# Optimization experiments

Measured on AMD Instinct MI355X. Metric: run time of the kernel, lower is better.

## Reference

```python
import jax, jax.numpy as jnp
import numpy as np

L, D, F, H = 4, 1024, 2048, 8
DH = D // H
EPS = 1e-5


def setup_inputs() -> dict:
    key = jax.random.key(0)
    ks = jax.random.split(key, 8)
    B, S = 4, 1024
    sd = 1.0 / np.sqrt(D)
    sf = 1.0 / np.sqrt(F)
    return {
        "X": jax.random.normal(ks[0], (B, S, D), jnp.float32),
        "Wq": jax.random.normal(ks[1], (L, D, D), jnp.float32) * sd,
        "Wk": jax.random.normal(ks[2], (L, D, D), jnp.float32) * sd,
        "Wv": jax.random.normal(ks[3], (L, D, D), jnp.float32) * sd,
        "Wg": jax.random.normal(ks[4], (L, D, D), jnp.float32) * sd,
        "Wo": jax.random.normal(ks[5], (L, D, D), jnp.float32) * sd,
        "W1": jax.random.normal(ks[6], (L, D, F), jnp.float32) * sd,
        "W2": jax.random.normal(ks[7], (L, F, D), jnp.float32) * sf,
        "ln_scale": jnp.ones((D,), jnp.float32),
        "ln_bias": jnp.zeros((D,), jnp.float32),
        "gn_scale": jnp.ones((L, D), jnp.float32),
        "gn_bias": jnp.zeros((L, D), jnp.float32),
    }


def _layer_norm(x, scale, bias):
    mu = x.mean(-1, keepdims=True)
    var = x.var(-1, keepdims=True)
    return (x - mu) * jax.lax.rsqrt(var + EPS) * scale + bias


def _rotate(x, cos, sin):
    # x: (B,S,H,DH); cos/sin: (1,S,1,DH//2); rotary pairs (even, odd)
    x1, x2 = x[..., 0::2], x[..., 1::2]
    r1 = x1 * cos - x2 * sin
    r2 = x1 * sin + x2 * cos
    return jnp.stack([r1, r2], axis=-1).reshape(x.shape)


def _decay_matrix(S):
    # D[h,n,m] = gamma_h^(n-m) for n>=m else 0
    gammas = 1.0 - jnp.exp(jnp.linspace(np.log(1 / 32), np.log(1 / 512), H)).astype(jnp.float32)
    n = jnp.arange(S)
    diff = (n[:, None] - n[None, :]).astype(jnp.float32)
    pw = jnp.exp(jnp.clip(diff, 0.0)[None] * jnp.log(gammas)[:, None, None])
    return jnp.where(diff[None] >= 0, pw, 0.0)  # (H,S,S)


def _retention(x, Wq, Wk, Wv, Wg, Wo, gn_s, gn_b, Dm, cos, sin):
    B, S, _ = x.shape
    Q = (x @ Wq).reshape(B, S, H, DH)
    K = (x @ Wk).reshape(B, S, H, DH)
    V = (x @ Wv).reshape(B, S, H, DH)
    Q = _rotate(Q, cos, sin)
    K = _rotate(K, cos, -sin)  # conjugate phase
    att = jnp.einsum('bnhd,bmhd->bhnm', Q, K) * Dm  # (B,H,S,S)
    Y = jnp.einsum('bhnm,bmhd->bnhd', att, V)
    # group norm: normalize each head's output per token
    mu = Y.mean(-1, keepdims=True)
    var = Y.var(-1, keepdims=True)
    Y = (Y - mu) * jax.lax.rsqrt(var + EPS)
    Y = Y.reshape(B, S, D) * gn_s + gn_b
    G = jax.nn.swish(x @ Wg)
    return (G * Y) @ Wo


def reference(X, Wq, Wk, Wv, Wg, Wo, W1, W2, ln_scale, ln_bias, gn_scale, gn_bias):
    B, S, _ = X.shape
    pos = jnp.arange(S, dtype=jnp.float32)
    inv_freq = 1.0 / (10000.0 ** (jnp.arange(0, DH, 2, dtype=jnp.float32) / DH))
    ang = pos[:, None] * inv_freq[None, :]  # (S, DH//2)
    cos = jnp.cos(ang)[None, :, None, :]
    sin = jnp.sin(ang)[None, :, None, :]
    Dm = _decay_matrix(S)
    for i in range(L):
        Yr = _retention(_layer_norm(X, ln_scale, ln_bias), Wq[i], Wk[i], Wv[i],
                        Wg[i], Wo[i], gn_scale[i], gn_bias[i], Dm, cos, sin) + X
        X = jax.nn.gelu(_layer_norm(Yr, ln_scale, ln_bias) @ W1[i]) @ W2[i] + Yr
    return X
```

## Files before the change

kernel.cpp:

```cpp
#include <hip/hip_runtime.h>
#include <hip/hip_bf16.h>
#include <cmath>

#define LAYERS 4
#define Bb 4
#define Ss 1024
#define Dd 1024
#define Ff 2048
#define Hh 8
#define DHd 128
#define Mm (Bb * Ss)
#define EPSf 1e-5f
#define LDQ 4096

typedef __attribute__((ext_vector_type(8))) short short8v;
typedef __attribute__((ext_vector_type(4))) float f32x4;
typedef __attribute__((ext_vector_type(4))) unsigned int u32x4;

__device__ __forceinline__ float swish_f(float x) { return x / (1.f + expf(-x)); }
__device__ __forceinline__ float gelu_f(float x) {
  return 0.5f * x * (1.f + tanhf(0.7978845608028654f * (x + 0.044715f * x * x * x)));
}
__device__ __forceinline__ unsigned short f2bfu(float f) {
  __hip_bfloat16 h = __float2bfloat16(f);
  return __builtin_bit_cast(unsigned short, h);
}
__device__ __forceinline__ float bfu2f(unsigned short u) {
  unsigned v = ((unsigned)u) << 16;
  return __builtin_bit_cast(float, v);
}
__device__ __forceinline__ void gl_lds16(const void* g, void* l) {
  __builtin_amdgcn_global_load_lds((__attribute__((address_space(1))) void*)g,
                                   (__attribute__((address_space(3))) void*)l, 16, 0, 0);
}
__device__ __forceinline__ f32x4 mfma16(short8v a, short8v b, f32x4 c) {
  return __builtin_amdgcn_mfma_f32_16x16x32_bf16(a, b, c, 0, 0, 0);
}

__global__ __launch_bounds__(256) void ln_bf16_kernel(const float* __restrict__ x,
                                                      short* __restrict__ outb,
                                                      const float* __restrict__ sc,
                                                      const float* __restrict__ bi) {
  const int row = blockIdx.x;
  const int t = threadIdx.x;
  const float4 v = *(const float4*)(x + (size_t)row * Dd + t * 4);
  float s = v.x + v.y + v.z + v.w;
  float s2 = v.x * v.x + v.y * v.y + v.z * v.z + v.w * v.w;
#pragma unroll
  for (int o = 32; o > 0; o >>= 1) { s += __shfl_down(s, o); s2 += __shfl_down(s2, o); }
  __shared__ float ps[4], ps2[4];
  if ((t & 63) == 0) { ps[t >> 6] = s; ps2[t >> 6] = s2; }
  __syncthreads();
  s = ps[0] + ps[1] + ps[2] + ps[3];
  s2 = ps2[0] + ps2[1] + ps2[2] + ps2[3];
  const float mu = s * (1.f / Dd);
  const float var = s2 * (1.f / Dd) - mu * mu;
  const float rstd = rsqrtf(var + EPSf);
  const float4 g = *(const float4*)(sc + t * 4);
  const float4 b = *(const float4*)(bi + t * 4);
  const float o0 = (v.x - mu) * rstd * g.x + b.x;
  const float o1 = (v.y - mu) * rstd * g.y + b.y;
  const float o2 = (v.z - mu) * rstd * g.z + b.z;
  const float o3 = (v.w - mu) * rstd * g.w + b.w;
  unsigned p0 = (unsigned)f2bfu(o0) | ((unsigned)f2bfu(o1) << 16);
  unsigned p1 = (unsigned)f2bfu(o2) | ((unsigned)f2bfu(o3) << 16);
  uint2 pk; pk.x = p0; pk.y = p1;
  *(uint2*)(outb + (size_t)row * Dd + t * 4) = pk;
}

__global__ void rope_table_kernel(float* __restrict__ ct, float* __restrict__ st) {
  const int i = blockIdx.x * 256 + threadIdx.x;
  const int s = i >> 6, f = i & 63;
  const float inv = powf(10000.f, -(float)f / 64.f);
  const float a = (float)s * inv;
  ct[i] = cosf(a);
  st[i] = sinf(a);
}

__global__ __launch_bounds__(256) void wtrans_all_kernel(
    const float* __restrict__ Wq, const float* __restrict__ Wk,
    const float* __restrict__ Wv, const float* __restrict__ Wg,
    const float* __restrict__ Wo, const float* __restrict__ W1,
    const float* __restrict__ W2,
    short* __restrict__ Wqkvgt, short* __restrict__ Wot,
    short* __restrict__ W1t, short* __restrict__ W2t) {
  __shared__ float tile[32][33];
  const int t = threadIdx.x;
  const int tc = t & 31, tr8 = t >> 5;
  const int blk = blockIdx.x;
  const float* src; short* dst; int K, N, n0, k0, nl;
  if (blk < 4096) {
    const int bx = blk & 127, ky = blk >> 7;
    n0 = bx * 32; k0 = ky * 32;
    const int which = n0 >> 10;
    src = (which == 0) ? Wq : (which == 1) ? Wk : (which == 2) ? Wv : Wg;
    nl = n0 & 1023; N = 1024; K = 1024; dst = Wqkvgt;
  } else if (blk < 5120) {
    const int b2 = blk - 4096;
    n0 = (b2 & 31) * 32; k0 = (b2 >> 5) * 32; nl = n0;
    src = Wo; N = 1024; K = 1024; dst = Wot;
  } else if (blk < 7168) {
    const int b2 = blk - 5120;
    n0 = (b2 & 63) * 32; k0 = (b2 >> 6) * 32; nl = n0;
    src = W1; N = 2048; K = 1024; dst = W1t;
  } else {
    const int b2 = blk - 7168;
    n0 = (b2 & 31) * 32; k0 = (b2 >> 5) * 32; nl = n0;
    src = W2; N = 1024; K = 2048; dst = W2t;
  }
#pragma unroll
  for (int i = 0; i < 4; ++i) {
    const int r = tr8 + i * 8;
    tile[r][tc] = src[(size_t)(k0 + r) * N + nl + tc];
  }
  __syncthreads();
#pragma unroll
  for (int i = 0; i < 4; ++i) {
    const int r = tr8 + i * 8;
    dst[(size_t)(n0 + r) * K + k0 + tc] = (short)f2bfu(tile[tc][r]);
  }
}

__global__ __launch_bounds__(256) void rvt_kernel(short* __restrict__ QKVGb,
                                                  short* __restrict__ Vt,
                                                  const float* __restrict__ ct,
                                                  const float* __restrict__ st) {
  __shared__ short tile[32][33];
  const int blk = blockIdx.x, t = threadIdx.x;
  if (blk < 8192) {
    const int idx = blk * 256 + t;
    const int f = idx & 63;
    const int h = (idx >> 6) & 7;
    const int r = idx >> 9;
    const int s = r & (Ss - 1);
    const float c = ct[(s << 6) + f], sn = st[(s << 6) + f];
    const size_t qo = (size_t)r * LDQ + h * DHd + 2 * f;
    const unsigned qp = *(const unsigned*)(QKVGb + qo);
    const unsigned kp = *(const unsigned*)(QKVGb + qo + 1024);
    const float qx = bfu2f((unsigned short)(qp & 0xffff)), qy = bfu2f((unsigned short)(qp >> 16));
    const float kx = bfu2f((unsigned short)(kp & 0xffff)), ky = bfu2f((unsigned short)(kp >> 16));
    const unsigned qn = (unsigned)f2bfu(qx * c - qy * sn) |
                        ((unsigned)f2bfu(qx * sn + qy * c) << 16);
    const unsigned kn = (unsigned)f2bfu(kx * c + ky * sn) |
                        ((unsigned)f2bfu(-kx * sn + ky * c) << 16);
    *(unsigned*)(QKVGb + qo) = qn;
    *(unsigned*)(QKVGb + qo + 1024) = kn;
  } else {
    const int vb = blk - 8192;
    const int s0 = (vb & 31) * 32, d0 = ((vb >> 5) & 3) * 32, bh = vb >> 7;
    const int bb = bh >> 3, h = bh & 7;
    const int tc = t & 31, tr8 = t >> 5;
#pragma unroll
    for (int i = 0; i < 4; ++i) {
      const int r = tr8 + i * 8;
      tile[r][tc] = QKVGb[(size_t)(bb * Ss + s0 + r) * LDQ + 2048 + h * DHd + d0 + tc];
    }
    __syncthreads();
#pragma unroll
    for (int i = 0; i < 4; ++i) {
      const int r = tr8 + i * 8;
      Vt[(size_t)(bh * DHd + d0 + r) * Ss + s0 + tc] = tile[tc][r];
    }
  }
}

template <int EPI>
__global__ __launch_bounds__(512, 2) void gemm14(const short* __restrict__ A,
                                                 const short* __restrict__ Bt,
                                                 float* __restrict__ Cf,
                                                 short* __restrict__ Cb,
                                                 const float* __restrict__ Res,
                                                 int N, int K, int ldc) {
  __shared__ __align__(16) short As[2][2][128 * 64];
  __shared__ __align__(16) short Bs[2][2][128 * 64];
  const int t = threadIdx.x;
  const int w = t >> 6, l = t & 63;
  const int lq = l >> 4, lr = l & 15;
  const int wr = w >> 2, wc = w & 3;
  const int bhalf = wc >> 1, brow0 = (wc & 1) * 64;
  const int nwg = gridDim.x * gridDim.y;
  const int bid0 = blockIdx.x + blockIdx.y * gridDim.x;
  const int lgid = (bid0 & 7) * (nwg >> 3) + (bid0 >> 3);
  const int bx = lgid % gridDim.x, by = lgid / gridDim.x;
  const int row0 = by * 256, col0 = bx * 256;
  const int NT = K >> 6;

  f32x4 acc[8][4] = {};
  short8v a[4][2], b[4][2];

  auto stageA = [&](int kt, int hf) {
    const int db = kt & 1;
#pragma unroll
    for (int i = 0; i < 2; ++i) {
      const int c = t + i * 512;
      const int row = c >> 3, slot = c & 7;
      gl_lds16(A + (size_t)(row0 + hf * 128 + row) * K + kt * 64 + ((slot ^ (row & 7)) << 3),
               &As[db][hf][c * 8]);
    }
  };
  auto stageB = [&](int kt, int hf) {
    const int db = kt & 1;
#pragma unroll
    for (int i = 0; i < 2; ++i) {
      const int c = t + i * 512;
      const int row = c >> 3, slot = c & 7;
      gl_lds16(Bt + (size_t)(col0 + hf * 128 + row) * K + kt * 64 + ((slot ^ (row & 7)) << 3),
               &Bs[db][hf][c * 8]);
    }
  };
  auto rdA = [&](int db, int m, int ks) -> short8v {
    const int row = m * 16 + lr;
    return *(const short8v*)&As[db][wr][row * 64 + (((ks << 2) + lq) ^ (row & 7)) * 8];
  };
  auto rdB = [&](int db, int n, int ks) -> short8v {
    const int row = brow0 + n * 16 + lr;
    return *(const short8v*)&Bs[db][bhalf][row * 64 + (((ks << 2) + lq) ^ (row & 7)) * 8];
  };

  stageA(0, 0); stageA(0, 1); stageB(0, 0); stageB(0, 1);
  if (NT > 1) { stageB(1, 0); stageB(1, 1); }
  if (NT > 1) { asm volatile("s_waitcnt vmcnt(4)" ::: "memory"); }
  else        { asm volatile("s_waitcnt vmcnt(0)" ::: "memory"); }
  asm volatile("s_barrier" ::: "memory");

  for (int kt = 0; kt < NT; ++kt) {
    const int db = kt & 1;
#pragma unroll
    for (int m = 0; m < 4; ++m) a[m][0] = rdA(db, m, 0);
#pragma unroll
    for (int n = 0; n < 4; ++n) b[n][0] = rdB(db, n, 0);
    if (kt + 1 < NT) stageA(kt + 1, 0);
    __builtin_amdgcn_s_setprio(1);
#pragma unroll
    for (int m = 0; m < 4; ++m)
#pragma unroll
      for (int n = 0; n < 4; ++n) acc[m][n] = mfma16(a[m][0], b[n][0], acc[m][n]);
    __builtin_amdgcn_s_setprio(0);
    asm volatile("s_barrier" ::: "memory");
#pragma unroll
    for (int m = 0; m < 4; ++m) a[m][1] = rdA(db, m, 1);
#pragma unroll
    for (int n = 0; n < 4; ++n) b[n][1] = rdB(db, n, 1);
    if (kt + 1 < NT) stageA(kt + 1, 1);
    __builtin_amdgcn_s_setprio(1);
#pragma unroll
    for (int m = 0; m < 4; ++m)
#pragma unroll
      for (int n = 0; n < 4; ++n) acc[m][n] = mfma16(a[m][1], b[n][1], acc[m][n]);
    __builtin_amdgcn_s_setprio(0);
    asm volatile("s_barrier" ::: "memory");
#pragma unroll
    for (int m = 0; m < 4; ++m) a[m][0] = rdA(db, m + 4, 0);
    if (kt + 2 < NT) { stageB(kt + 2, 0); stageB(kt + 2, 1); }
    __builtin_amdgcn_s_setprio(1);
#pragma unroll
    for (int m = 0; m < 4; ++m)
#pragma unroll
      for (int n = 0; n < 4; ++n) acc[m + 4][n] = mfma16(a[m][0], b[n][0], acc[m + 4][n]);
    __builtin_amdgcn_s_setprio(0);
    asm volatile("s_barrier" ::: "memory");
#pragma unroll
    for (int m = 0; m < 4; ++m) a[m][1] = rdA(db, m + 4, 1);
    __builtin_amdgcn_s_setprio(1);
#pragma unroll
    for (int m = 0; m < 4; ++m)
#pragma unroll
      for (int n = 0; n < 4; ++n) acc[m + 4][n] = mfma16(a[m][1], b[n][1], acc[m + 4][n]);
    __builtin_amdgcn_s_setprio(0);
    if (kt + 2 < NT) { asm volatile("s_waitcnt vmcnt(4)" ::: "memory"); }
    else             { asm volatile("s_waitcnt vmcnt(0)" ::: "memory"); }
    asm volatile("s_barrier" ::: "memory");
  }

#pragma unroll
  for (int m = 0; m < 8; ++m) {
#pragma unroll
    for (int n = 0; n < 4; ++n) {
#pragma unroll
      for (int r = 0; r < 4; ++r) {
        const int row = row0 + wr * 128 + m * 16 + lq * 4 + r;
        const int col = col0 + wc * 64 + n * 16 + lr;
        const size_t o = (size_t)row * ldc + col;
        float v = acc[m][n][r];
        if (EPI == 0) Cb[o] = (short)f2bfu(v);
        else if (EPI == 1) Cf[o] = v + Res[o];
        else Cb[o] = (short)f2bfu(gelu_f(v));
      }
    }
  }
}

template <int EPI>
__global__ __launch_bounds__(512) void gemm11(const short* __restrict__ A,
                                              const short* __restrict__ Bt,
                                              float* __restrict__ Cf,
                                              short* __restrict__ Cb,
                                              const float* __restrict__ Res,
                                              int K, int lda, int ldb, int ldc, int nxt) {
  __shared__ __align__(16) short As[3][256 * 64];
  __shared__ __align__(16) short Bs[3][128 * 64];
  const int t = threadIdx.x;
  const int w = t >> 6, l = t & 63;
  const int lq = l >> 4, lr = l & 15;
  const int wr = w >> 2, wc = w & 3;
  const int nwg = gridDim.x;
  const int lgid = (blockIdx.x & 7) * (nwg >> 3) + (blockIdx.x >> 3);
  const int mt = lgid / nxt, nt_ = lgid % nxt;
  const int row0 = mt * 256, col0 = nt_ * 128;
  const int NT = K >> 6;
  f32x4 acc[8][2] = {};
  short8v a[4][2], b[2][2];

  auto stageA = [&](int kt, int hf) {
    const int s = kt % 3;
#pragma unroll
    for (int i = 0; i < 2; ++i) {
      const int c = t + i * 512;
      const int row = c >> 3, slot = c & 7;
      gl_lds16(A + (size_t)(row0 + hf * 128 + row) * lda + kt * 64 + ((slot ^ (row & 7)) << 3),
               &As[s][hf * 8192 + c * 8]);
    }
  };
  auto stageB = [&](int kt) {
    const int s = kt % 3;
#pragma unroll
    for (int i = 0; i < 2; ++i) {
      const int c = t + i * 512;
      const int row = c >> 3, slot = c & 7;
      gl_lds16(Bt + (size_t)(col0 + row) * ldb + kt * 64 + ((slot ^ (row & 7)) << 3),
               &Bs[s][c * 8]);
    }
  };
  auto rdA = [&](int s, int m, int ks) -> short8v {
    const int row = wr * 128 + m * 16 + lr;
    return *(const short8v*)&As[s][row * 64 + (((ks << 2) + lq) ^ (row & 7)) * 8];
  };
  auto rdB = [&](int s, int n, int ks) -> short8v {
    const int row = wc * 32 + n * 16 + lr;
    return *(const short8v*)&Bs[s][row * 64 + (((ks << 2) + lq) ^ (row & 7)) * 8];
  };

  stageA(0, 0); stageA(0, 1); stageB(0);
  stageA(1, 0); stageA(1, 1); stageB(1);
  asm volatile("s_waitcnt vmcnt(6)" ::: "memory");
  asm volatile("s_barrier" ::: "memory");

  for (int kt = 0; kt < NT; ++kt) {
    const int s = kt % 3;
#pragma unroll
    for (int m = 0; m < 4; ++m) { a[m][0] = rdA(s, m, 0); a[m][1] = rdA(s, m, 1); }
#pragma unroll
    for (int n = 0; n < 2; ++n) { b[n][0] = rdB(s, n, 0); b[n][1] = rdB(s, n, 1); }
    if (kt + 2 < NT) stageA(kt + 2, 0);
    __builtin_amdgcn_s_setprio(1);
#pragma unroll
    for (int m = 0; m < 4; ++m)
#pragma unroll
      for (int n = 0; n < 2; ++n) {
        acc[m][n] = mfma16(a[m][0], b[n][0], acc[m][n]);
        acc[m][n] = mfma16(a[m][1], b[n][1], acc[m][n]);
      }
    __builtin_amdgcn_s_setprio(0);
    asm volatile("s_barrier" ::: "memory");
#pragma unroll
    for (int m = 0; m < 4; ++m) { a[m][0] = rdA(s, m + 4, 0); a[m][1] = rdA(s, m + 4, 1); }
    if (kt + 2 < NT) { stageA(kt + 2, 1); stageB(kt + 2); }
    __builtin_amdgcn_s_setprio(1);
#pragma unroll
    for (int m = 0; m < 4; ++m)
#pragma unroll
      for (int n = 0; n < 2; ++n) {
        acc[m + 4][n] = mfma16(a[m][0], b[n][0], acc[m + 4][n]);
        acc[m + 4][n] = mfma16(a[m][1], b[n][1], acc[m + 4][n]);
      }
    __builtin_amdgcn_s_setprio(0);
    if (kt + 2 < NT) { asm volatile("s_waitcnt vmcnt(6)" ::: "memory"); }
    else             { asm volatile("s_waitcnt vmcnt(0)" ::: "memory"); }
    asm volatile("s_barrier" ::: "memory");
  }

#pragma unroll
  for (int m = 0; m < 8; ++m) {
#pragma unroll
    for (int n = 0; n < 2; ++n) {
#pragma unroll
      for (int r = 0; r < 4; ++r) {
        const int row = row0 + wr * 128 + m * 16 + lq * 4 + r;
        const int col = col0 + wc * 32 + n * 16 + lr;
        const size_t o = (size_t)row * ldc + col;
        float v = acc[m][n][r];
        if (EPI == 0) Cb[o] = (short)f2bfu(v);
        else if (EPI == 1) Cf[o] = v + Res[o];
        else Cb[o] = (short)f2bfu(gelu_f(v));
      }
    }
  }
}

template <int EPI>
__global__ __launch_bounds__(512) void gemm12(const short* __restrict__ A,
                                              const short* __restrict__ Bt,
                                              float* __restrict__ Cf,
                                              short* __restrict__ Cb,
                                              const float* __restrict__ Res,
                                              int K, int lda, int ldb, int ldc, int nxt) {
  __shared__ __align__(16) short As[3][128 * 64];
  __shared__ __align__(16) short Bs[3][128 * 64];
  const int t = threadIdx.x;
  const int w = t >> 6, l = t & 63;
  const int lq = l >> 4, lr = l & 15;
  const int wr = w >> 2, wc = w & 3;
  const int nwg = gridDim.x;
  const int lgid = (blockIdx.x & 7) * (nwg >> 3) + (blockIdx.x >> 3);
  const int mt = lgid / nxt, nt_ = lgid % nxt;
  const int row0 = mt * 128, col0 = nt_ * 128;
  const int NT = K >> 6;
  f32x4 acc[4][2] = {};
  short8v a[4][2], b[2][2];

  auto stageA = [&](int kt) {
    const int s = kt % 3;
#pragma unroll
    for (int i = 0; i < 2; ++i) {
      const int c = t + i * 512;
      const int row = c >> 3, slot = c & 7;
      gl_lds16(A + (size_t)(row0 + row) * lda + kt * 64 + ((slot ^ (row & 7)) << 3),
               &As[s][c * 8]);
    }
  };
  auto stageB = [&](int kt) {
    const int s = kt % 3;
#pragma unroll
    for (int i = 0; i < 2; ++i) {
      const int c = t + i * 512;
      const int row = c >> 3, slot = c & 7;
      gl_lds16(Bt + (size_t)(col0 + row) * ldb + kt * 64 + ((slot ^ (row & 7)) << 3),
               &Bs[s][c * 8]);
    }
  };
  auto rdA = [&](int s, int m, int ks) -> short8v {
    const int row = wr * 64 + m * 16 + lr;
    return *(const short8v*)&As[s][row * 64 + (((ks << 2) + lq) ^ (row & 7)) * 8];
  };
  auto rdB = [&](int s, int n, int ks) -> short8v {
    const int row = wc * 32 + n * 16 + lr;
    return *(const short8v*)&Bs[s][row * 64 + (((ks << 2) + lq) ^ (row & 7)) * 8];
  };

  stageA(0); stageB(0);
  stageA(1); stageB(1);
  asm volatile("s_waitcnt vmcnt(4)" ::: "memory");
  asm volatile("s_barrier" ::: "memory");

  for (int kt = 0; kt < NT; ++kt) {
    const int s = kt % 3;
#pragma unroll
    for (int m = 0; m < 4; ++m) { a[m][0] = rdA(s, m, 0); a[m][1] = rdA(s, m, 1); }
#pragma unroll
    for (int n = 0; n < 2; ++n) { b[n][0] = rdB(s, n, 0); b[n][1] = rdB(s, n, 1); }
    if (kt + 2 < NT) stageA(kt + 2);
    __builtin_amdgcn_s_setprio(1);
#pragma unroll
    for (int m = 0; m < 2; ++m)
#pragma unroll
      for (int n = 0; n < 2; ++n) {
        acc[m][n] = mfma16(a[m][0], b[n][0], acc[m][n]);
        acc[m][n] = mfma16(a[m][1], b[n][1], acc[m][n]);
      }
    __builtin_amdgcn_s_setprio(0);
    asm volatile("s_barrier" ::: "memory");
    if (kt + 2 < NT) stageB(kt + 2);
    __builtin_amdgcn_s_setprio(1);
#pragma unroll
    for (int m = 2; m < 4; ++m)
#pragma unroll
      for (int n = 0; n < 2; ++n) {
        acc[m][n] = mfma16(a[m][0], b[n][0], acc[m][n]);
        acc[m][n] = mfma16(a[m][1], b[n][1], acc[m][n]);
      }
    __builtin_amdgcn_s_setprio(0);
    if (kt + 2 < NT) { asm volatile("s_waitcnt vmcnt(4)" ::: "memory"); }
    else             { asm volatile("s_waitcnt vmcnt(0)" ::: "memory"); }
    asm volatile("s_barrier" ::: "memory");
  }

#pragma unroll
  for (int m = 0; m < 4; ++m) {
#pragma unroll
    for (int n = 0; n < 2; ++n) {
#pragma unroll
      for (int r = 0; r < 4; ++r) {
        const int row = row0 + wr * 64 + m * 16 + lq * 4 + r;
        const int col = col0 + wc * 32 + n * 16 + lr;
        const size_t o = (size_t)row * ldc + col;
        float v = acc[m][n][r];
        if (EPI == 0) Cb[o] = (short)f2bfu(v);
        else if (EPI == 1) Cf[o] = v + Res[o];
        else Cb[o] = (short)f2bfu(gelu_f(v));
      }
    }
  }
}

__global__ __launch_bounds__(256) void ret4_kernel(const short* __restrict__ QKb,
                                                   const short* __restrict__ Vt,
                                                   float* __restrict__ Y0,
                                                   float* __restrict__ Y1) {
  __shared__ __align__(16) short Ks[2][64 * 128];
  __shared__ __align__(16) short Vs[2][128 * 64];
  const int t = threadIdx.x, w = t >> 6, l = t & 63;
  const int lq = l >> 4, lr = l & 15;
  const int u = blockIdx.x;
  const int lgid = (u & 7) * 64 + (u >> 3);
  const int half = lgid >> 8;
  const int rest = lgid & 255;
  const int bh = rest >> 3, j = rest & 7;
  const int qb = half ? j : 7 - j;
  const int b = bh >> 3, h = bh & 7;
  const int q0 = qb * 128;
  const float lstep = (logf(1.f / 512.f) - logf(1.f / 32.f)) * (1.f / 7.f);
  const float gamma = 1.f - expf(logf(1.f / 32.f) + (float)h * lstep);
  const float l2g = logf(gamma) * 1.44269504f;
  const short* Qp = QKb;
  const short* Kp = QKb + 1024;

  short8v qf[2][4];
#pragma unroll
  for (int qn = 0; qn < 2; ++qn)
#pragma unroll
    for (int ks = 0; ks < 4; ++ks)
      qf[qn][ks] = *(const short8v*)(Qp + (size_t)(b * Ss + q0 + w * 32 + qn * 16 + lr) * LDQ +
                                     h * DHd + ks * 32 + lq * 8);

  float cmf[4], csr[4];
#pragma unroll
  for (int mf = 0; mf < 4; ++mf) cmf[mf] = exp2f(l2g * (float)(-16 * mf));
#pragma unroll
  for (int r = 0; r < 4; ++r) csr[r] = exp2f(l2g * (float)(63 - 4 * lq - r));

  f32x4 yacc[2][8] = {};
  const int nt = 2 * qb + 2;
  const int sb = ((lq & 1) * 2) * 16 + lr;

  auto stageKV = [&](int m0, int buf) {
#pragma unroll
    for (int i = 0; i < 4; ++i) {
      const int c = (w * 4 + i) * 64 + l;
      const int row = c >> 4, slot = c & 15;
      gl_lds16(Kp + (size_t)(b * Ss + m0 + row) * LDQ + h * DHd + ((slot ^ (row & 7)) * 8),
               &Ks[buf][(w * 4 + i) * 512]);
    }
#pragma unroll
    for (int i = 0; i < 4; ++i) {
      const int c = (w * 4 + i) * 64 + l;
      const int row = c >> 3, slot = c & 7;
      gl_lds16(Vt + (size_t)(bh * DHd + row) * Ss + m0 + ((slot ^ (row & 7)) * 8),
               &Vs[buf][(w * 4 + i) * 512]);
    }
  };

  stageKV(half * 64, 0);
  __syncthreads();
  int cur = 0;
  for (int tt = half; tt < nt; tt += 2) {
    const int m0 = tt * 64;
    if (tt + 2 < nt) stageKV((tt + 2) * 64, cur ^ 1);

    f32x4 st[4][2] = {};
    __builtin_amdgcn_s_setprio(1);
#pragma unroll
    for (int mf = 0; mf < 4; ++mf) {
      const int row = mf * 16 + lr;
#pragma unroll
      for (int ks = 0; ks < 4; ++ks) {
        short8v kf = *(const short8v*)&Ks[cur][row * 128 + (((4 * ks + lq) ^ (row & 7)) * 8)];
        st[mf][0] = mfma16(kf, qf[0][ks], st[mf][0]);
        st[mf][1] = mfma16(kf, qf[1][ks], st[mf][1]);
      }
    }
    __builtin_amdgcn_s_setprio(0);
    float rs[2];
#pragma unroll
    for (int qn = 0; qn < 2; ++qn)
      rs[qn] = exp2f(l2g * (float)(q0 + w * 32 + qn * 16 + lr - m0 - 63));
#pragma unroll
    for (int mf = 0; mf < 4; ++mf)
#pragma unroll
      for (int qn = 0; qn < 2; ++qn)
#pragma unroll
        for (int r = 0; r < 4; ++r) {
          const int qg = q0 + w * 32 + qn * 16 + lr;
          const int kvg = m0 + mf * 16 + lq * 4 + r;
          const float wgt = (qg >= kvg) ? rs[qn] * cmf[mf] * csr[r] : 0.f;
          st[mf][qn][r] *= wgt;
        }
    unsigned pk[4][2][2];
#pragma unroll
    for (int mf = 0; mf < 4; ++mf)
#pragma unroll
      for (int qn = 0; qn < 2; ++qn)
#pragma unroll
        for (int p = 0; p < 2; ++p)
          pk[mf][qn][p] = (unsigned)f2bfu(st[mf][qn][2 * p]) |
                          ((unsigned)f2bfu(st[mf][qn][2 * p + 1]) << 16);
    short8v afr[2][2];
#pragma unroll
    for (int qn = 0; qn < 2; ++qn)
#pragma unroll
      for (int ks2 = 0; ks2 < 2; ++ks2) {
        u32x4 wd;
#pragma unroll
        for (int wj = 0; wj < 4; ++wj) {
          const int src = sb + (wj >> 1) * 16;
          const unsigned v0 = __shfl(pk[2 * ks2 + 0][qn][wj & 1], src);
          const unsigned v1 = __shfl(pk[2 * ks2 + 1][qn][wj & 1], src);
          wd[wj] = (lq >= 2) ? v1 : v0;
        }
        afr[qn][ks2] = __builtin_bit_cast(short8v, wd);
      }
    __builtin_amdgcn_s_setprio(1);
#pragma unroll
    for (int nd = 0; nd < 8; ++nd) {
      const int row = nd * 16 + lr;
#pragma unroll
      for (int ks2 = 0; ks2 < 2; ++ks2) {
        short8v vf = *(const short8v*)&Vs[cur][row * 64 + (((4 * ks2 + lq) ^ (row & 7)) * 8)];
        yacc[0][nd] = mfma16(afr[0][ks2], vf, yacc[0][nd]);
        yacc[1][nd] = mfma16(afr[1][ks2], vf, yacc[1][nd]);
      }
    }
    __builtin_amdgcn_s_setprio(0);
    __syncthreads();
    cur ^= 1;
  }
  float* Y = half ? Y1 : Y0;
#pragma unroll
  for (int qn = 0; qn < 2; ++qn)
#pragma unroll
    for (int r = 0; r < 4; ++r) {
      const int q = q0 + w * 32 + qn * 16 + lq * 4 + r;
#pragma unroll
      for (int nd = 0; nd < 8; ++nd)
        Y[(size_t)(b * Ss + q) * Dd + h * DHd + nd * 16 + lr] = yacc[qn][nd][r];
    }
}

__global__ __launch_bounds__(256) void gate_kernel(const float* __restrict__ Y0,
                                                   const float* __restrict__ Y1,
                                                   const short* __restrict__ Graw,
                                                   short* __restrict__ Gb,
                                                   const float* __restrict__ gs,
                                                   const float* __restrict__ gb) {
  const int lane = threadIdx.x & 63;
  const int rowh = blockIdx.x * 4 + (threadIdx.x >> 6);
  const int h = rowh & 7;
  const int row = rowh >> 3;
  const size_t ybase = (size_t)row * Dd + (size_t)h * DHd + lane * 2;
  float2 a = *(const float2*)(Y0 + ybase);
  const float2 c = *(const float2*)(Y1 + ybase);
  a.x += c.x; a.y += c.y;
  float s = a.x + a.y, s2 = a.x * a.x + a.y * a.y;
#pragma unroll
  for (int o = 32; o > 0; o >>= 1) { s += __shfl_down(s, o); s2 += __shfl_down(s2, o); }
  s = __shfl(s, 0);
  s2 = __shfl(s2, 0);
  const float mu = s * (1.f / DHd);
  const float rstd = rsqrtf(s2 * (1.f / DHd) - mu * mu + EPSf);
  const int d = h * DHd + lane * 2;
  const float2 g = *(const float2*)(gs + d);
  const float2 bbv = *(const float2*)(gb + d);
  const float y0 = (a.x - mu) * rstd * g.x + bbv.x;
  const float y1 = (a.y - mu) * rstd * g.y + bbv.y;
  const unsigned gr = *(const unsigned*)(Graw + (size_t)row * LDQ + 3072 + h * DHd + lane * 2);
  const float gx = bfu2f((unsigned short)(gr & 0xffff));
  const float gy = bfu2f((unsigned short)(gr >> 16));
  const unsigned o01 = (unsigned)f2bfu(swish_f(gx) * y0) |
                       ((unsigned)f2bfu(swish_f(gy) * y1) << 16);
  *(unsigned*)(Gb + ybase) = o01;
}

extern "C" void kernel_launch(void* const* d_in, const int* in_sizes, int n_in,
                              void* d_out, int out_size, void* d_ws, size_t ws_size,
                              hipStream_t stream) {
  const float* X = (const float*)d_in[0];
  const float* Wq = (const float*)d_in[1];
  const float* Wk = (const float*)d_in[2];
  const float* Wv = (const float*)d_in[3];
  const float* Wg = (const float*)d_in[4];
  const float* Wo = (const float*)d_in[5];
  const float* W1 = (const float*)d_in[6];
  const float* W2 = (const float*)d_in[7];
  const float* lns = (const float*)d_in[8];
  const float* lnb = (const float*)d_in[9];
  const float* gns = (const float*)d_in[10];
  const float* gnb = (const float*)d_in[11];
  float* out = (float*)d_out;

  char* W = (char*)d_ws;
  const size_t MB = 1u << 20;
  float* Abuf  = (float*)(W);
  short* Xnb   = (short*)(W + 16 * MB);
  short* QKVGb = (short*)(W + 24 * MB);
  float* Y0    = (float*)(W + 56 * MB);
  float* Y1    = (float*)(W + 72 * MB);
  short* Vtb   = (short*)(W + 88 * MB);
  short* Gb    = (short*)(W + 96 * MB);
  short* Wqkvgt= (short*)(W + 104 * MB);
  short* Wot   = (short*)(W + 112 * MB);
  short* W1t   = (short*)(W + 114 * MB);
  short* W2t   = (short*)(W + 118 * MB);
  float* ct    = (float*)(W + 122 * MB);
  float* st    = ct + Ss * 64;
  short* Hb = QKVGb;

  rope_table_kernel<<<(Ss * 64) / 256, 256, 0, stream>>>(ct, st);

  for (int l = 0; l < LAYERS; ++l) {
    const size_t DD = (size_t)Dd * Dd;
    const float* Acur = (l == 0) ? X : Abuf;
    wtrans_all_kernel<<<9216, 256, 0, stream>>>(Wq + l * DD, Wk + l * DD, Wv + l * DD,
                                                Wg + l * DD, Wo + l * DD,
                                                W1 + (size_t)l * Dd * Ff,
                                                W2 + (size_t)l * Ff * Dd,
                                                Wqkvgt, Wot, W1t, W2t);
    ln_bf16_kernel<<<Mm, 256, 0, stream>>>(Acur, Xnb, lns, lnb);
    gemm14<0><<<dim3(16, 16), 512, 0, stream>>>(Xnb, Wqkvgt, nullptr, QKVGb,
                                                nullptr, 4096, Dd, LDQ);
    rvt_kernel<<<12288, 256, 0, stream>>>(QKVGb, Vtb, ct, st);
    ret4_kernel<<<512, 256, 0, stream>>>(QKVGb, Vtb, Y0, Y1);
    gate_kernel<<<(Mm * Hh) / 4, 256, 0, stream>>>(Y0, Y1, QKVGb, Gb,
                                                   gns + (size_t)l * Dd, gnb + (size_t)l * Dd);
    gemm12<1><<<256, 512, 0, stream>>>(Gb, Wot, Abuf, nullptr, Acur,
                                       Dd, Dd, Dd, Dd, 8);
    ln_bf16_kernel<<<Mm, 256, 0, stream>>>(Abuf, Xnb, lns, lnb);
    gemm11<2><<<256, 512, 0, stream>>>(Xnb, W1t, nullptr, Hb, nullptr,
                                       Dd, Dd, Dd, Ff, 16);
    float* dst = (l == LAYERS - 1) ? out : Abuf;
    gemm12<1><<<256, 512, 0, stream>>>(Hb, W2t, dst, nullptr, Abuf,
                                       Ff, Ff, Ff, Dd, 8);
  }
}
```

Baseline: 746.7 us.

## Fuse retention with group-norm gating and add explicit barriers in QKVG GEMM

```diff
diff --git a/kernel.cpp b/kernel.cpp
--- a/kernel.cpp
+++ b/kernel.cpp
@@ -230,6 +230,9 @@
 #pragma unroll
     for (int n = 0; n < 4; ++n) b[n][0] = rdB(db, n, 0);
     if (kt + 1 < NT) stageA(kt + 1, 0);
+    asm volatile("s_barrier" ::: "memory");
+    asm volatile("s_waitcnt lgkmcnt(0)" ::: "memory");
+    __builtin_amdgcn_sched_barrier(0);
     __builtin_amdgcn_s_setprio(1);
 #pragma unroll
     for (int m = 0; m < 4; ++m)
@@ -242,6 +245,9 @@
 #pragma unroll
     for (int n = 0; n < 4; ++n) b[n][1] = rdB(db, n, 1);
     if (kt + 1 < NT) stageA(kt + 1, 1);
+    asm volatile("s_barrier" ::: "memory");
+    asm volatile("s_waitcnt lgkmcnt(0)" ::: "memory");
+    __builtin_amdgcn_sched_barrier(0);
     __builtin_amdgcn_s_setprio(1);
 #pragma unroll
     for (int m = 0; m < 4; ++m)
@@ -252,6 +258,9 @@
 #pragma unroll
     for (int m = 0; m < 4; ++m) a[m][0] = rdA(db, m + 4, 0);
     if (kt + 2 < NT) { stageB(kt + 2, 0); stageB(kt + 2, 1); }
+    asm volatile("s_barrier" ::: "memory");
+    asm volatile("s_waitcnt lgkmcnt(0)" ::: "memory");
+    __builtin_amdgcn_sched_barrier(0);
     __builtin_amdgcn_s_setprio(1);
 #pragma unroll
     for (int m = 0; m < 4; ++m)
@@ -261,6 +270,9 @@
     asm volatile("s_barrier" ::: "memory");
 #pragma unroll
     for (int m = 0; m < 4; ++m) a[m][1] = rdA(db, m + 4, 1);
+    asm volatile("s_barrier" ::: "memory");
+    asm volatile("s_waitcnt lgkmcnt(0)" ::: "memory");
+    __builtin_amdgcn_sched_barrier(0);
     __builtin_amdgcn_s_setprio(1);
 #pragma unroll
     for (int m = 0; m < 4; ++m)
@@ -502,44 +514,36 @@
   }
 }
 
-__global__ __launch_bounds__(256) void ret4_kernel(const short* __restrict__ QKb,
+__global__ __launch_bounds__(256) void ret5_kernel(const short* __restrict__ QKVGb,
                                                    const short* __restrict__ Vt,
-                                                   float* __restrict__ Y0,
-                                                   float* __restrict__ Y1) {
+                                                   short* __restrict__ Gb,
+                                                   const float* __restrict__ gs,
+                                                   const float* __restrict__ gb) {
   __shared__ __align__(16) short Ks[2][64 * 128];
   __shared__ __align__(16) short Vs[2][128 * 64];
   const int t = threadIdx.x, w = t >> 6, l = t & 63;
   const int lq = l >> 4, lr = l & 15;
   const int u = blockIdx.x;
-  const int lgid = (u & 7) * 64 + (u >> 3);
-  const int half = lgid >> 8;
-  const int rest = lgid & 255;
-  const int bh = rest >> 3, j = rest & 7;
-  const int qb = half ? j : 7 - j;
+  const int lgid = (u & 7) * 32 + (u >> 3);
+  const int bh = lgid >> 3, pr = lgid & 7;
   const int b = bh >> 3, h = bh & 7;
-  const int q0 = qb * 128;
   const float lstep = (logf(1.f / 512.f) - logf(1.f / 32.f)) * (1.f / 7.f);
   const float gamma = 1.f - expf(logf(1.f / 32.f) + (float)h * lstep);
   const float l2g = logf(gamma) * 1.44269504f;
-  const short* Qp = QKb;
-  const short* Kp = QKb + 1024;
-
-  short8v qf[2][4];
-#pragma unroll
-  for (int qn = 0; qn < 2; ++qn)
-#pragma unroll
-    for (int ks = 0; ks < 4; ++ks)
-      qf[qn][ks] = *(const short8v*)(Qp + (size_t)(b * Ss + q0 + w * 32 + qn * 16 + lr) * LDQ +
-                                     h * DHd + ks * 32 + lq * 8);
+  const short* Qp = QKVGb;
+  const short* Kp = QKVGb + 1024;
 
   float cmf[4], csr[4];
 #pragma unroll
   for (int mf = 0; mf < 4; ++mf) cmf[mf] = exp2f(l2g * (float)(-16 * mf));
 #pragma unroll
   for (int r = 0; r < 4; ++r) csr[r] = exp2f(l2g * (float)(63 - 4 * lq - r));
-
-  f32x4 yacc[2][8] = {};
-  const int nt = 2 * qb + 2;
+  float gsv[8], gbv[8];
+#pragma unroll
+  for (int nd = 0; nd < 8; ++nd) {
+    gsv[nd] = gs[h * DHd + nd * 16 + lr];
+    gbv[nd] = gb[h * DHd + nd * 16 + lr];
+  }
   const int sb = ((lq & 1) * 2) * 16 + lr;
 
   auto stageKV = [&](int m0, int buf) {
@@ -559,124 +563,103 @@
     }
   };
 
-  stageKV(half * 64, 0);
-  __syncthreads();
-  int cur = 0;
-  for (int tt = half; tt < nt; tt += 2) {
-    const int m0 = tt * 64;
-    if (tt + 2 < nt) stageKV((tt + 2) * 64, cur ^ 1);
-
-    f32x4 st[4][2] = {};
-    __builtin_amdgcn_s_setprio(1);
-#pragma unroll
-    for (int mf = 0; mf < 4; ++mf) {
-      const int row = mf * 16 + lr;
-#pragma unroll
-      for (int ks = 0; ks < 4; ++ks) {
-        short8v kf = *(const short8v*)&Ks[cur][row * 128 + (((4 * ks + lq) ^ (row & 7)) * 8)];
-        st[mf][0] = mfma16(kf, qf[0][ks], st[mf][0]);
-        st[mf][1] = mfma16(kf, qf[1][ks], st[mf][1]);
-      }
-    }
-    __builtin_amdgcn_s_setprio(0);
-    float rs[2];
-#pragma unroll
-    for (int qn = 0; qn < 2; ++qn)
-      rs[qn] = exp2f(l2g * (float)(q0 + w * 32 + qn * 16 + lr - m0 - 63));
-#pragma unroll
-    for (int mf = 0; mf < 4; ++mf)
-#pragma unroll
-      for (int qn = 0; qn < 2; ++qn)
+  for (int pass = 0; pass < 2; ++pass) {
+    const int qb = pass ? (15 - pr) : pr;
+    const int q0 = qb * 64;
+    const int nt = qb + 1;
+    short8v qf[4];
+#pragma unroll
+    for (int ks = 0; ks < 4; ++ks)
+      qf[ks] = *(const short8v*)(Qp + (size_t)(b * Ss + q0 + w * 16 + lr) * LDQ +
+                                 h * DHd + ks * 32 + lq * 8);
+    f32x4 yacc[8] = {};
+    stageKV(0, 0);
+    __syncthreads();
+    int cur = 0;
+    for (int tt = 0; tt < nt; ++tt) {
+      const int m0 = tt * 64;
+      if (tt + 1 < nt) stageKV((tt + 1) * 64, cur ^ 1);
+
+      f32x4 st[4] = {};
+      __builtin_amdgcn_s_setprio(1);
+#pragma unroll
+      for (int mf = 0; mf < 4; ++mf) {
+        const int row = mf * 16 + lr;
+#pragma unroll
+        for (int ks = 0; ks < 4; ++ks) {
+          short8v kf = *(const short8v*)&Ks[cur][row * 128 + (((4 * ks + lq) ^ (row & 7)) * 8)];
+          st[mf] = mfma16(kf, qf[ks], st[mf]);
+        }
+      }
+      __builtin_amdgcn_s_setprio(0);
+      const int qg = q0 + w * 16 + lr;
+      const float rs = exp2f(l2g * (float)(qg - m0 - 63));
+#pragma unroll
+      for (int mf = 0; mf < 4; ++mf)
 #pragma unroll
         for (int r = 0; r < 4; ++r) {
-          const int qg = q0 + w * 32 + qn * 16 + lr;
           const int kvg = m0 + mf * 16 + lq * 4 + r;
-          const float wgt = (qg >= kvg) ? rs[qn] * cmf[mf] * csr[r] : 0.f;
-          st[mf][qn][r] *= wgt;
+          const float wgt = (qg >= kvg) ? rs * cmf[mf] * csr[r] : 0.f;
+          st[mf][r] *= wgt;
         }
-    unsigned pk[4][2][2];
-#pragma unroll
-    for (int mf = 0; mf < 4; ++mf)
-#pragma unroll
-      for (int qn = 0; qn < 2; ++qn)
+      unsigned pk[4][2];
+#pragma unroll
+      for (int mf = 0; mf < 4; ++mf)
 #pragma unroll
         for (int p = 0; p < 2; ++p)
-          pk[mf][qn][p] = (unsigned)f2bfu(st[mf][qn][2 * p]) |
-                          ((unsigned)f2bfu(st[mf][qn][2 * p + 1]) << 16);
-    short8v afr[2][2];
-#pragma unroll
-    for (int qn = 0; qn < 2; ++qn)
+          pk[mf][p] = (unsigned)f2bfu(st[mf][2 * p]) |
+                      ((unsigned)f2bfu(st[mf][2 * p + 1]) << 16);
+      short8v afr[2];
 #pragma unroll
       for (int ks2 = 0; ks2 < 2; ++ks2) {
         u32x4 wd;
 #pragma unroll
         for (int wj = 0; wj < 4; ++wj) {
           const int src = sb + (wj >> 1) * 16;
-          const unsigned v0 = __shfl(pk[2 * ks2 + 0][qn][wj & 1], src);
-          const unsigned v1 = __shfl(pk[2 * ks2 + 1][qn][wj & 1], src);
+          const unsigned v0 = __shfl(pk[2 * ks2 + 0][wj & 1], src);
+          const unsigned v1 = __shfl(pk[2 * ks2 + 1][wj & 1], src);
           wd[wj] = (lq >= 2) ? v1 : v0;
         }
-        afr[qn][ks2] = __builtin_bit_cast(short8v, wd);
-      }
-    __builtin_amdgcn_s_setprio(1);
-#pragma unroll
-    for (int nd = 0; nd < 8; ++nd) {
-      const int row = nd * 16 + lr;
-#pragma unroll
-      for (int ks2 = 0; ks2 < 2; ++ks2) {
-        short8v vf = *(const short8v*)&Vs[cur][row * 64 + (((4 * ks2 + lq) ^ (row & 7)) * 8)];
-        yacc[0][nd] = mfma16(afr[0][ks2], vf, yacc[0][nd]);
-        yacc[1][nd] = mfma16(afr[1][ks2], vf, yacc[1][nd]);
-      }
-    }
-    __builtin_amdgcn_s_setprio(0);
-    __syncthreads();
-    cur ^= 1;
-  }
-  float* Y = half ? Y1 : Y0;
-#pragma unroll
-  for (int qn = 0; qn < 2; ++qn)
+        afr[ks2] = __builtin_bit_cast(short8v, wd);
+      }
+      __builtin_amdgcn_s_setprio(1);
+#pragma unroll
+      for (int nd = 0; nd < 8; ++nd) {
+        const int row = nd * 16 + lr;
+#pragma unroll
+        for (int ks2 = 0; ks2 < 2; ++ks2) {
+          short8v vf = *(const short8v*)&Vs[cur][row * 64 + (((4 * ks2 + lq) ^ (row & 7)) * 8)];
+          yacc[nd] = mfma16(afr[ks2], vf, yacc[nd]);
+        }
+      }
+      __builtin_amdgcn_s_setprio(0);
+      __syncthreads();
+      cur ^= 1;
+    }
 #pragma unroll
     for (int r = 0; r < 4; ++r) {
-      const int q = q0 + w * 32 + qn * 16 + lq * 4 + r;
-#pragma unroll
-      for (int nd = 0; nd < 8; ++nd)
-        Y[(size_t)(b * Ss + q) * Dd + h * DHd + nd * 16 + lr] = yacc[qn][nd][r];
-    }
-}
-
-__global__ __launch_bounds__(256) void gate_kernel(const float* __restrict__ Y0,
-                                                   const float* __restrict__ Y1,
-                                                   const short* __restrict__ Graw,
-                                                   short* __restrict__ Gb,
-                                                   const float* __restrict__ gs,
-                                                   const float* __restrict__ gb) {
-  const int lane = threadIdx.x & 63;
-  const int rowh = blockIdx.x * 4 + (threadIdx.x >> 6);
-  const int h = rowh & 7;
-  const int row = rowh >> 3;
-  const size_t ybase = (size_t)row * Dd + (size_t)h * DHd + lane * 2;
-  float2 a = *(const float2*)(Y0 + ybase);
-  const float2 c = *(const float2*)(Y1 + ybase);
-  a.x += c.x; a.y += c.y;
-  float s = a.x + a.y, s2 = a.x * a.x + a.y * a.y;
-#pragma unroll
-  for (int o = 32; o > 0; o >>= 1) { s += __shfl_down(s, o); s2 += __shfl_down(s2, o); }
-  s = __shfl(s, 0);
-  s2 = __shfl(s2, 0);
-  const float mu = s * (1.f / DHd);
-  const float rstd = rsqrtf(s2 * (1.f / DHd) - mu * mu + EPSf);
-  const int d = h * DHd + lane * 2;
-  const float2 g = *(const float2*)(gs + d);
-  const float2 bbv = *(const float2*)(gb + d);
-  const float y0 = (a.x - mu) * rstd * g.x + bbv.x;
-  const float y1 = (a.y - mu) * rstd * g.y + bbv.y;
-  const unsigned gr = *(const unsigned*)(Graw + (size_t)row * LDQ + 3072 + h * DHd + lane * 2);
-  const float gx = bfu2f((unsigned short)(gr & 0xffff));
-  const float gy = bfu2f((unsigned short)(gr >> 16));
-  const unsigned o01 = (unsigned)f2bfu(swish_f(gx) * y0) |
-                       ((unsigned)f2bfu(swish_f(gy) * y1) << 16);
-  *(unsigned*)(Gb + ybase) = o01;
+      float s1 = 0.f, s2 = 0.f;
+#pragma unroll
+      for (int nd = 0; nd < 8; ++nd) { const float v = yacc[nd][r]; s1 += v; s2 += v * v; }
+#pragma unroll
+      for (int msk = 1; msk < 16; msk <<= 1) {
+        s1 += __shfl_xor(s1, msk);
+        s2 += __shfl_xor(s2, msk);
+      }
+      const float mu = s1 * (1.f / 128.f);
+      const float rstd = rsqrtf(s2 * (1.f / 128.f) - mu * mu + EPSf);
+      const int q = q0 + w * 16 + lq * 4 + r;
+      const size_t gbase = (size_t)(b * Ss + q) * LDQ + 3072 + h * DHd;
+      const size_t obase = (size_t)(b * Ss + q) * Dd + h * DHd;
+#pragma unroll
+      for (int nd = 0; nd < 8; ++nd) {
+        const int d = nd * 16 + lr;
+        const float yv = (yacc[nd][r] - mu) * rstd * gsv[nd] + gbv[nd];
+        const float gvx = bfu2f((unsigned short)QKVGb[gbase + d]);
+        Gb[obase + d] = (short)f2bfu(swish_f(gvx) * yv);
+      }
+    }
+  }
 }
 
 extern "C" void kernel_launch(void* const* d_in, const int* in_sizes, int n_in,
@@ -701,8 +684,6 @@
   float* Abuf  = (float*)(W);
   short* Xnb   = (short*)(W + 16 * MB);
   short* QKVGb = (short*)(W + 24 * MB);
-  float* Y0    = (float*)(W + 56 * MB);
-  float* Y1    = (float*)(W + 72 * MB);
   short* Vtb   = (short*)(W + 88 * MB);
   short* Gb    = (short*)(W + 96 * MB);
   short* Wqkvgt= (short*)(W + 104 * MB);
@@ -727,9 +708,8 @@
     gemm14<0><<<dim3(16, 16), 512, 0, stream>>>(Xnb, Wqkvgt, nullptr, QKVGb,
                                                 nullptr, 4096, Dd, LDQ);
     rvt_kernel<<<12288, 256, 0, stream>>>(QKVGb, Vtb, ct, st);
-    ret4_kernel<<<512, 256, 0, stream>>>(QKVGb, Vtb, Y0, Y1);
-    gate_kernel<<<(Mm * Hh) / 4, 256, 0, stream>>>(Y0, Y1, QKVGb, Gb,
-                                                   gns + (size_t)l * Dd, gnb + (size_t)l * Dd);
+    ret5_kernel<<<256, 256, 0, stream>>>(QKVGb, Vtb, Gb,
+                                         gns + (size_t)l * Dd, gnb + (size_t)l * Dd);
     gemm12<1><<<256, 512, 0, stream>>>(Gb, Wot, Abuf, nullptr, Acur,
                                        Dd, Dd, Dd, Dd, 8);
     ln_bf16_kernel<<<Mm, 256, 0, stream>>>(Abuf, Xnb, lns, lnb);
```

Result: faster. 721.9 us (-3.3%).
